# Kernel tuning notes

Measured on AMD Instinct MI355X. Metric: run time of the kernel, lower is better.

The kernel has to match this reference:

```python
import jax, jax.numpy as jnp
import numpy as np

EMBED_DIM = 1024
NUM_HEADS = 16
HEAD_DIM = EMBED_DIM // NUM_HEADS
SCALE = 1.0 / np.sqrt(HEAD_DIM)


def _quant_linear(x, w, b):
    # Per-tensor symmetric int8 quantize -> dequantize -> GEMM (faithful to QuantizedLinear)
    s = jnp.max(jnp.abs(w)) / 127.0
    w_dq = jnp.clip(jnp.round(w / s), -128.0, 127.0) * s
    return jnp.einsum('bse,oe->bso', x, w_dq) + b


def setup_inputs() -> dict:
    key = jax.random.key(0)
    ks = jax.random.split(key, 7)
    B, S, E = 2, 2048, EMBED_DIM
    return {
        'query': jax.random.normal(ks[0], (B, S, E), dtype=jnp.float32),
        'key': jax.random.normal(ks[1], (B, S, E), dtype=jnp.float32),
        'value': jax.random.normal(ks[2], (B, S, E), dtype=jnp.float32),
        'Wq': jax.random.normal(ks[3], (E, E), dtype=jnp.float32) * 0.02,
        'bq': jnp.zeros((E,), dtype=jnp.float32),
        'Wk': jax.random.normal(ks[4], (E, E), dtype=jnp.float32) * 0.02,
        'bk': jnp.zeros((E,), dtype=jnp.float32),
        'Wv': jax.random.normal(ks[5], (E, E), dtype=jnp.float32) * 0.02,
        'bv': jnp.zeros((E,), dtype=jnp.float32),
        'Wo': jax.random.normal(ks[6], (E, E), dtype=jnp.float32) * 0.02,
        'bo': jnp.zeros((E,), dtype=jnp.float32),
    }


def reference(query, key, value, Wq, bq, Wk, bk, Wv, bv, Wo, bo):
    B, S, E = query.shape
    H, D = NUM_HEADS, HEAD_DIM
    Q = _quant_linear(query, Wq, bq).reshape(B, S, H, D).transpose(0, 2, 1, 3)
    K = _quant_linear(key, Wk, bk).reshape(B, S, H, D).transpose(0, 2, 1, 3)
    V = _quant_linear(value, Wv, bv).reshape(B, S, H, D).transpose(0, 2, 1, 3)
    # [B,H,S,S] unfused attention scores
    scores = jnp.einsum('bhqd,bhkd->bhqk', Q, K) * SCALE
    attn = jax.nn.softmax(scores, axis=-1)  # dropout is identity at inference
    out = jnp.einsum('bhqk,bhkd->bhqd', attn, V)
    out = out.transpose(0, 2, 1, 3).reshape(B, S, E)
    return _quant_linear(out, Wo, bo)
```

## Files before the change

kernel.cpp:

```cpp
#include <hip/hip_runtime.h>
#include <math.h>

#define S_LEN 2048
#define EMB   1024
#define NHEAD 16
#define HDIM  64
#define MTOT  4096
#define EXP2_SCALE 0.18033688011112042f

typedef __attribute__((ext_vector_type(8))) short bf16x8;
typedef __attribute__((ext_vector_type(4))) float f32x4;

#if __has_builtin(__builtin_amdgcn_exp2f)
#define FEXP2(x) __builtin_amdgcn_exp2f(x)
#else
#define FEXP2(x) exp2f(x)
#endif

__device__ __forceinline__ short f2bf(float f) {
  union { float f; unsigned u; } v; v.f = f;
  unsigned r = v.u + 0x7fffu + ((v.u >> 16) & 1u);
  return (short)(r >> 16);
}
__device__ __forceinline__ float bf2f(short s) {
  union { float f; unsigned u; } v; v.u = ((unsigned)(unsigned short)s) << 16;
  return v.f;
}
__device__ __forceinline__ unsigned pkbf(float e0, float e1) {
  unsigned a = __float_as_uint(e1) + 0x8000u;
  unsigned b = __float_as_uint(e0) + 0x8000u;
  return __builtin_amdgcn_perm(a, b, 0x07060302u);
}

__device__ __forceinline__ void gload_lds16(const void* g, void* l) {
  __builtin_amdgcn_global_load_lds(
      (const __attribute__((address_space(1))) void*)g,
      (__attribute__((address_space(3))) void*)l, 16, 0, 0);
}

__global__ void wabsmax_k(const float* __restrict__ W0, const float* __restrict__ W1,
                          const float* __restrict__ W2, const float* __restrict__ W3,
                          unsigned* __restrict__ scaleU) {
  int w = blockIdx.x & 3;
  int part = blockIdx.x >> 2;
  const float* W = (w == 0) ? W0 : (w == 1) ? W1 : (w == 2) ? W2 : W3;
  float m = 0.f;
  int base = part * 16384;
#pragma unroll
  for (int p = 0; p < 16; ++p) {
    const float4 v = *(const float4*)&W[base + p * 1024 + threadIdx.x * 4];
    m = fmaxf(m, fmaxf(fmaxf(fabsf(v.x), fabsf(v.y)), fmaxf(fabsf(v.z), fabsf(v.w))));
  }
  __shared__ float red[256];
  red[threadIdx.x] = m;
  __syncthreads();
  for (int s = 128; s > 0; s >>= 1) {
    if (threadIdx.x < s) red[threadIdx.x] = fmaxf(red[threadIdx.x], red[threadIdx.x + s]);
    __syncthreads();
  }
  if (threadIdx.x == 0) atomicMax(&scaleU[w], __float_as_uint(red[0]));
}

__global__ void wquant_k(const float* __restrict__ W0, const float* __restrict__ W1,
                         const float* __restrict__ W2, const float* __restrict__ W3,
                         short* __restrict__ Q0, short* __restrict__ Q1,
                         short* __restrict__ Q2, short* __restrict__ Q3,
                         const unsigned* __restrict__ scaleU, float* __restrict__ sVal) {
  int w = blockIdx.y;
  const float* W = (w == 0) ? W0 : (w == 1) ? W1 : (w == 2) ? W2 : W3;
  short* Q = (w == 0) ? Q0 : (w == 1) ? Q1 : (w == 2) ? Q2 : Q3;
  float s = __uint_as_float(scaleU[w]) * (1.0f / 127.0f);
  if (blockIdx.x == 0 && threadIdx.x == 0) sVal[w] = s;
  int idx = (blockIdx.x * 256 + threadIdx.x) * 4;
  float4 v = *(const float4*)&W[idx];
  short4 q;
  q.x = f2bf(fminf(fmaxf(rintf(v.x / s), -128.f), 127.f));
  q.y = f2bf(fminf(fmaxf(rintf(v.y / s), -128.f), 127.f));
  q.z = f2bf(fminf(fmaxf(rintf(v.z / s), -128.f), 127.f));
  q.w = f2bf(fminf(fmaxf(rintf(v.w / s), -128.f), 127.f));
  *(short4*)&Q[idx] = q;
}

__global__ void acast_k(const float* __restrict__ A0, const float* __restrict__ A1,
                        const float* __restrict__ A2,
                        short* __restrict__ H0, short* __restrict__ H1,
                        short* __restrict__ H2) {
  int w = blockIdx.y;
  const float* A = (w == 0) ? A0 : (w == 1) ? A1 : A2;
  short* H = (w == 0) ? H0 : (w == 1) ? H1 : H2;
  int idx = (blockIdx.x * 256 + threadIdx.x) * 4;
  float4 v = *(const float4*)&A[idx];
  short4 h;
  h.x = f2bf(v.x); h.y = f2bf(v.y); h.z = f2bf(v.z); h.w = f2bf(v.w);
  *(short4*)&H[idx] = h;
}

__device__ __forceinline__ void gemm_core(
    const short* __restrict__ Ah, const short* __restrict__ Bq, int m0, int n0,
    short* AhS, short* BsS, f32x4 acc[4][4]) {
  const int tid = threadIdx.x;
  const int lane = tid & 63, wave = tid >> 6;
  const int quad = lane >> 4, l16 = lane & 15;
  const int wm = wave >> 1, wn = wave & 1;

  const int swrow = lane >> 2, swcol = (lane & 3) * 8;
  const short* agh = Ah + (m0 + wave * 32 + swrow) * 1024 + swcol;
  const short* bgp = Bq + (n0 + wave * 32 + swrow) * 1024 + swcol;
  short* sA0 = AhS + wave * 1024;
  short* sB0 = BsS + wave * 1024;

  for (int k0 = 0; k0 < 1024; k0 += 32) {
    __syncthreads();
    gload_lds16(agh + k0,             sA0);
    gload_lds16(agh + 16 * 1024 + k0, sA0 + 512);
    gload_lds16(bgp + k0,             sB0);
    gload_lds16(bgp + 16 * 1024 + k0, sB0 + 512);
    __syncthreads();
    bf16x8 ah[4], bb[4];
#pragma unroll
    for (int mi = 0; mi < 4; ++mi) {
      int row = wm * 64 + mi * 16 + l16;
      ah[mi] = *(const bf16x8*)&AhS[row * 32 + quad * 8];
    }
#pragma unroll
    for (int ni = 0; ni < 4; ++ni) {
      int row = wn * 64 + ni * 16 + l16;
      bb[ni] = *(const bf16x8*)&BsS[row * 32 + quad * 8];
    }
#pragma unroll
    for (int mi = 0; mi < 4; ++mi)
#pragma unroll
      for (int ni = 0; ni < 4; ++ni)
        acc[mi][ni] = __builtin_amdgcn_mfma_f32_16x16x32_bf16(ah[mi], bb[ni], acc[mi][ni], 0, 0, 0);
  }
}

__global__ __launch_bounds__(256, 2) void gemm_qkv(
    const short* __restrict__ QA, const short* __restrict__ KA, const short* __restrict__ VA,
    const short* __restrict__ WqQ, const short* __restrict__ WkQ, const short* __restrict__ WvQ,
    const float* __restrict__ sVal,
    const float* __restrict__ bq, const float* __restrict__ bk, const float* __restrict__ bv,
    short* __restrict__ Qh, short* __restrict__ Kh, short* __restrict__ Vh) {
  __shared__ __align__(16) short AhS[128 * 32];
  __shared__ __align__(16) short BsS[128 * 32];
  const int z = blockIdx.z;
  const short* Ah = (z == 0) ? QA : (z == 1) ? KA : VA;
  const short* Bq = (z == 0) ? WqQ : (z == 1) ? WkQ : WvQ;
  const float* bias = (z == 0) ? bq : (z == 1) ? bk : bv;
  short* oh = (z == 0) ? Qh : (z == 1) ? Kh : Vh;

  const int lin = blockIdx.y * 8 + blockIdx.x;
  const int map = (lin & 7) * 32 + (lin >> 3);
  const int m0 = (map >> 3) * 128, n0 = (map & 7) * 128;
  f32x4 acc[4][4];
#pragma unroll
  for (int i = 0; i < 4; ++i)
#pragma unroll
    for (int j = 0; j < 4; ++j) acc[i][j] = (f32x4){0.f, 0.f, 0.f, 0.f};

  gemm_core(Ah, Bq, m0, n0, AhS, BsS, acc);

  const int lane = threadIdx.x & 63, wave = threadIdx.x >> 6;
  const int quad = lane >> 4, l16 = lane & 15;
  const int wm = wave >> 1, wn = wave & 1;
  float s = sVal[z];
  float post = (z == 0) ? EXP2_SCALE : 1.0f;
#pragma unroll
  for (int mi = 0; mi < 4; ++mi) {
#pragma unroll
    for (int ni = 0; ni < 4; ++ni) {
      int rowb = m0 + wm * 64 + mi * 16 + quad * 4;
      int col = n0 + wn * 64 + ni * 16 + l16;
      float bia = bias[col];
      int h = col >> 6, d = col & 63;
      if (z < 2) {
#pragma unroll
        for (int r = 0; r < 4; ++r) {
          float v = (acc[mi][ni][r] * s + bia) * post;
          int row = rowb + r;
          int b = row >> 11, sq = row & 2047;
          oh[((b * 16 + h) * 2048 + sq) * 64 + d] = f2bf(v);
        }
      } else {
        int b = rowb >> 11, sq = rowb & 2047;
        short4 pk;
        pk.x = f2bf(acc[mi][ni][0] * s + bia);
        pk.y = f2bf(acc[mi][ni][1] * s + bia);
        pk.z = f2bf(acc[mi][ni][2] * s + bia);
        pk.w = f2bf(acc[mi][ni][3] * s + bia);
        *(short4*)&oh[((b * 16 + h) * 64 + d) * 2048 + sq] = pk;
      }
    }
  }
}

__global__ __launch_bounds__(256, 2) void gemm_o(
    const short* __restrict__ OAh, const short* __restrict__ OAl,
    const short* __restrict__ WoQ, const float* __restrict__ sPtr,
    const float* __restrict__ bias, float* __restrict__ outF) {
  __shared__ __align__(16) short AhS[128 * 32];
  __shared__ __align__(16) short AlS[128 * 32];
  __shared__ __align__(16) short BsS[64 * 32];
  const int tid = threadIdx.x;
  const int lane = tid & 63, wave = tid >> 6;
  const int quad = lane >> 4, l16 = lane & 15;
  const int lin = blockIdx.y * 16 + blockIdx.x;
  const int map = (lin & 7) * 64 + (lin >> 3);
  const int m0 = (map >> 4) * 128, n0 = (map & 15) * 64;

  f32x4 acc[2][4];
#pragma unroll
  for (int i = 0; i < 2; ++i)
#pragma unroll
    for (int j = 0; j < 4; ++j) acc[i][j] = (f32x4){0.f, 0.f, 0.f, 0.f};

  const int swrow = lane >> 2, swcol = (lane & 3) * 8;
  const short* agh = OAh + (m0 + wave * 32 + swrow) * 1024 + swcol;
  const short* agl = OAl + (m0 + wave * 32 + swrow) * 1024 + swcol;
  const short* bgp = WoQ + (n0 + wave * 16 + swrow) * 1024 + swcol;
  short* sA0 = AhS + wave * 1024;
  short* sA1 = AlS + wave * 1024;
  short* sB0 = BsS + wave * 512;

  for (int k0 = 0; k0 < 1024; k0 += 32) {
    __syncthreads();
    gload_lds16(agh + k0,             sA0);
    gload_lds16(agh + 16 * 1024 + k0, sA0 + 512);
    gload_lds16(agl + k0,             sA1);
    gload_lds16(agl + 16 * 1024 + k0, sA1 + 512);
    gload_lds16(bgp + k0,             sB0);
    __syncthreads();
    bf16x8 ah[2], al[2], bb[4];
#pragma unroll
    for (int mi = 0; mi < 2; ++mi) {
      int row = wave * 32 + mi * 16 + l16;
      ah[mi] = *(const bf16x8*)&AhS[row * 32 + quad * 8];
      al[mi] = *(const bf16x8*)&AlS[row * 32 + quad * 8];
    }
#pragma unroll
    for (int ni = 0; ni < 4; ++ni) {
      int row = ni * 16 + l16;
      bb[ni] = *(const bf16x8*)&BsS[row * 32 + quad * 8];
    }
#pragma unroll
    for (int mi = 0; mi < 2; ++mi)
#pragma unroll
      for (int ni = 0; ni < 4; ++ni) {
        acc[mi][ni] = __builtin_amdgcn_mfma_f32_16x16x32_bf16(ah[mi], bb[ni], acc[mi][ni], 0, 0, 0);
        acc[mi][ni] = __builtin_amdgcn_mfma_f32_16x16x32_bf16(al[mi], bb[ni], acc[mi][ni], 0, 0, 0);
      }
  }

  const float s = *sPtr;
#pragma unroll
  for (int mi = 0; mi < 2; ++mi) {
#pragma unroll
    for (int ni = 0; ni < 4; ++ni) {
      int rowb = m0 + wave * 32 + mi * 16 + quad * 4;
      int col = n0 + ni * 16 + l16;
      float bia = bias[col];
#pragma unroll
      for (int r = 0; r < 4; ++r)
        outF[(rowb + r) * 1024 + col] = acc[mi][ni][r] * s + bia;
    }
  }
}

__global__ __launch_bounds__(256, 2) void flash_k(
    const short* __restrict__ Qh, const short* __restrict__ Kh,
    const short* __restrict__ Vh,
    short* __restrict__ Ohi, short* __restrict__ Olo) {
  __shared__ __align__(16) short Khs[64 * 72];
  __shared__ __align__(16) short Vhs[64 * 72];

  const int tid = threadIdx.x;
  const int lane = tid & 63, wave = tid >> 6;
  const int quad = lane >> 4, l16 = lane & 15;
  const int bh = blockIdx.y;
  const int b = bh >> 4, h = bh & 15;
  const int q0 = blockIdx.x * 128 + wave * 32;
  const int qkbase = bh * (S_LEN * HDIM);
  const int vbase  = bh * (HDIM * S_LEN);

  bf16x8 qb[2][2];
#pragma unroll
  for (int g = 0; g < 2; ++g) {
    const int qrow = qkbase + (q0 + g * 16 + l16) * HDIM;
    qb[g][0] = *(const bf16x8*)&Qh[qrow + quad * 8];
    qb[g][1] = *(const bf16x8*)&Qh[qrow + 32 + quad * 8];
  }

  f32x4 zero = {0.f, 0.f, 0.f, 0.f};
  f32x4 oacc[2][4];
#pragma unroll
  for (int g = 0; g < 2; ++g)
#pragma unroll
    for (int i = 0; i < 4; ++i) oacc[g][i] = zero;
  f32x4 sacc[2] = {zero, zero};

  union { bf16x8 v; unsigned u[4]; } ones_;
  ones_.u[0] = ones_.u[1] = ones_.u[2] = ones_.u[3] = 0x3F803F80u;

  const int sr  = wave * 16 + l16;
  const int sc8 = quad * 8;
  const int srP = (sr & 32) | (((sr >> 2) & 1) << 4) | (((sr >> 3) & 3) << 2) | (sr & 3);
  const int kgl = qkbase + sr * HDIM + sc8;
  const int vgl = vbase + sr * S_LEN + sc8;
  const int kOff = srP * 72 + sc8;
  const int vOff = sr * 72 + sc8;

  bf16x8 pk0 = *(const bf16x8*)&Kh[kgl];
  bf16x8 pk1 = *(const bf16x8*)&Kh[kgl + 32];
  bf16x8 pv0 = *(const bf16x8*)&Vh[vgl];
  bf16x8 pv1 = *(const bf16x8*)&Vh[vgl + 32];

  for (int kt = 0; kt < S_LEN; kt += 64) {
    __syncthreads();
    *(bf16x8*)&Khs[kOff]      = pk0;
    *(bf16x8*)&Khs[kOff + 32] = pk1;
    *(bf16x8*)&Vhs[vOff]      = pv0;
    *(bf16x8*)&Vhs[vOff + 32] = pv1;
    __syncthreads();
    if (kt + 64 < S_LEN) {
      int kg = kgl + (kt + 64) * HDIM;
      int vg = vgl + (kt + 64);
      pk0 = *(const bf16x8*)&Kh[kg];
      pk1 = *(const bf16x8*)&Kh[kg + 32];
      pv0 = *(const bf16x8*)&Vh[vg];
      pv1 = *(const bf16x8*)&Vh[vg + 32];
    }
    f32x4 sc[2][4];
#pragma unroll
    for (int nj = 0; nj < 4; ++nj) {
      const int kr = nj * 16 + l16;
      bf16x8 kf0 = *(const bf16x8*)&Khs[kr * 72 + quad * 8];
      bf16x8 kf1 = *(const bf16x8*)&Khs[kr * 72 + 32 + quad * 8];
#pragma unroll
      for (int g = 0; g < 2; ++g) {
        f32x4 sv = zero;
        sv = __builtin_amdgcn_mfma_f32_16x16x32_bf16(kf0, qb[g][0], sv, 0, 0, 0);
        sv = __builtin_amdgcn_mfma_f32_16x16x32_bf16(kf1, qb[g][1], sv, 0, 0, 0);
        sc[g][nj] = sv;
      }
    }
#pragma unroll
    for (int g = 0; g < 2; ++g)
#pragma unroll
      for (int nj = 0; nj < 4; ++nj)
#pragma unroll
        for (int r = 0; r < 4; ++r)
          sc[g][nj][r] = FEXP2(sc[g][nj][r]);
    union { bf16x8 v; unsigned u[4]; } P[2][2];
#pragma unroll
    for (int g = 0; g < 2; ++g) {
      P[g][0].u[0] = pkbf(sc[g][0][0], sc[g][0][1]);
      P[g][0].u[1] = pkbf(sc[g][0][2], sc[g][0][3]);
      P[g][0].u[2] = pkbf(sc[g][1][0], sc[g][1][1]);
      P[g][0].u[3] = pkbf(sc[g][1][2], sc[g][1][3]);
      P[g][1].u[0] = pkbf(sc[g][2][0], sc[g][2][1]);
      P[g][1].u[1] = pkbf(sc[g][2][2], sc[g][2][3]);
      P[g][1].u[2] = pkbf(sc[g][3][0], sc[g][3][1]);
      P[g][1].u[3] = pkbf(sc[g][3][2], sc[g][3][3]);
    }
#pragma unroll
    for (int g = 0; g < 2; ++g) {
      sacc[g] = __builtin_amdgcn_mfma_f32_16x16x32_bf16(P[g][0].v, ones_.v, sacc[g], 0, 0, 0);
      sacc[g] = __builtin_amdgcn_mfma_f32_16x16x32_bf16(P[g][1].v, ones_.v, sacc[g], 0, 0, 0);
    }
#pragma unroll
    for (int ni = 0; ni < 4; ++ni) {
      int vr = ni * 16 + l16;
      bf16x8 vf0 = *(const bf16x8*)&Vhs[vr * 72 + quad * 8];
      bf16x8 vf1 = *(const bf16x8*)&Vhs[vr * 72 + 32 + quad * 8];
#pragma unroll
      for (int g = 0; g < 2; ++g) {
        oacc[g][ni] = __builtin_amdgcn_mfma_f32_16x16x32_bf16(P[g][0].v, vf0, oacc[g][ni], 0, 0, 0);
        oacc[g][ni] = __builtin_amdgcn_mfma_f32_16x16x32_bf16(P[g][1].v, vf1, oacc[g][ni], 0, 0, 0);
      }
    }
  }
#pragma unroll
  for (int g = 0; g < 2; ++g) {
#pragma unroll
    for (int r = 0; r < 4; ++r) {
      float inv = 1.f / sacc[g][r];
      int row = b * S_LEN + q0 + g * 16 + quad * 4 + r;
#pragma unroll
      for (int ni = 0; ni < 4; ++ni) {
        float v = oacc[g][ni][r] * inv;
        int idx = row * 1024 + h * 64 + ni * 16 + l16;
        short hi = f2bf(v);
        Ohi[idx] = hi;
        Olo[idx] = f2bf(v - bf2f(hi));
      }
    }
  }
}

extern "C" void kernel_launch(void* const* d_in, const int* in_sizes, int n_in,
                              void* d_out, int out_size, void* d_ws, size_t ws_size,
                              hipStream_t stream) {
  const float* query = (const float*)d_in[0];
  const float* key_i = (const float*)d_in[1];
  const float* value = (const float*)d_in[2];
  const float* Wq = (const float*)d_in[3];
  const float* bq = (const float*)d_in[4];
  const float* Wk = (const float*)d_in[5];
  const float* bk = (const float*)d_in[6];
  const float* Wv = (const float*)d_in[7];
  const float* bv = (const float*)d_in[8];
  const float* Wo = (const float*)d_in[9];
  const float* bo = (const float*)d_in[10];
  float* out = (float*)d_out;

  char* w = (char*)d_ws;
  unsigned* scaleU = (unsigned*)w;
  float* sVal = (float*)(w + 256);
  size_t off = 512;
  const size_t SZ_W = 2097152;
  const size_t SZ_A = 8388608;
  short* WqQ = (short*)(w + off); off += SZ_W;
  short* WkQ = (short*)(w + off); off += SZ_W;
  short* WvQ = (short*)(w + off); off += SZ_W;
  short* WoQ = (short*)(w + off); off += SZ_W;
  short* Qa  = (short*)(w + off); off += SZ_A;
  short* Ka  = (short*)(w + off); off += SZ_A;
  short* Va  = (short*)(w + off); off += SZ_A;
  short* Qh  = (short*)(w + off); off += SZ_A;
  short* Kh  = (short*)(w + off); off += SZ_A;
  short* Vh  = (short*)(w + off); off += SZ_A;
  short* Ohi = Qa;
  short* Olo = Ka;

  (void)hipMemsetAsync(scaleU, 0, 16, stream);
  wabsmax_k<<<256, 256, 0, stream>>>(Wq, Wk, Wv, Wo, scaleU);
  wquant_k<<<dim3(1024, 4), 256, 0, stream>>>(Wq, Wk, Wv, Wo, WqQ, WkQ, WvQ, WoQ, scaleU, sVal);
  acast_k<<<dim3(4096, 3), 256, 0, stream>>>(query, key_i, value, Qa, Ka, Va);
  gemm_qkv<<<dim3(8, 32, 3), 256, 0, stream>>>(Qa, Ka, Va, WqQ, WkQ, WvQ, sVal,
                                               bq, bk, bv, Qh, Kh, Vh);
  flash_k<<<dim3(16, 32), 256, 0, stream>>>(Qh, Kh, Vh, Ohi, Olo);
  gemm_o<<<dim3(16, 32), 256, 0, stream>>>(Ohi, Olo, WoQ, sVal + 3, bo, out);
}
```

Measured before the change: 233.3 us.

## Load K fragments directly from global into registers and remap block order

The flash attention kernel stops staging K through shared memory. Each lane instead loads its K MFMA fragments straight from global memory into double-buffered register sets, unrolling the loop by two tiles, and only V still goes through LDS. The block index is also remapped so that neighbouring blocks work on different heads, which is meant to spread L2 and cache traffic. This cuts LDS writes and reads for K, but every wave now re-reads K from global or L2 and register pressure goes up.

```diff
diff --git a/kernel.cpp b/kernel.cpp
--- a/kernel.cpp
+++ b/kernel.cpp
@@ -266,19 +266,95 @@
   }
 }
 
+#define MF(a, b, c) __builtin_amdgcn_mfma_f32_16x16x32_bf16(a, b, c, 0, 0, 0)
+
+#define FLASH_TILE(KF, KN, ktv)                                               \
+  {                                                                           \
+    __syncthreads();                                                          \
+    *(bf16x8*)&Vhs[vOff]      = pv0;                                          \
+    *(bf16x8*)&Vhs[vOff + 32] = pv1;                                          \
+    __syncthreads();                                                          \
+    const int ktn = (ktv) + 64;                                               \
+    if (ktn < S_LEN) {                                                        \
+      pv0 = *(const bf16x8*)&Vh[vgl + ktn];                                   \
+      pv1 = *(const bf16x8*)&Vh[vgl + ktn + 32];                              \
+      const int ko = ktn * HDIM;                                              \
+      KN##0 = *(const bf16x8*)&kp0[ko]; KN##1 = *(const bf16x8*)&kp0[ko + 32];\
+      KN##2 = *(const bf16x8*)&kp1[ko]; KN##3 = *(const bf16x8*)&kp1[ko + 32];\
+      KN##4 = *(const bf16x8*)&kp2[ko]; KN##5 = *(const bf16x8*)&kp2[ko + 32];\
+      KN##6 = *(const bf16x8*)&kp3[ko]; KN##7 = *(const bf16x8*)&kp3[ko + 32];\
+    }                                                                         \
+    f32x4 sc[2][4];                                                           \
+    {                                                                         \
+      f32x4 sv;                                                               \
+      sv = zero; sv = MF(KF##0, qb[0][0], sv); sv = MF(KF##1, qb[0][1], sv);  \
+      sc[0][0] = sv;                                                          \
+      sv = zero; sv = MF(KF##0, qb[1][0], sv); sv = MF(KF##1, qb[1][1], sv);  \
+      sc[1][0] = sv;                                                          \
+      sv = zero; sv = MF(KF##2, qb[0][0], sv); sv = MF(KF##3, qb[0][1], sv);  \
+      sc[0][1] = sv;                                                          \
+      sv = zero; sv = MF(KF##2, qb[1][0], sv); sv = MF(KF##3, qb[1][1], sv);  \
+      sc[1][1] = sv;                                                          \
+      sv = zero; sv = MF(KF##4, qb[0][0], sv); sv = MF(KF##5, qb[0][1], sv);  \
+      sc[0][2] = sv;                                                          \
+      sv = zero; sv = MF(KF##4, qb[1][0], sv); sv = MF(KF##5, qb[1][1], sv);  \
+      sc[1][2] = sv;                                                          \
+      sv = zero; sv = MF(KF##6, qb[0][0], sv); sv = MF(KF##7, qb[0][1], sv);  \
+      sc[0][3] = sv;                                                          \
+      sv = zero; sv = MF(KF##6, qb[1][0], sv); sv = MF(KF##7, qb[1][1], sv);  \
+      sc[1][3] = sv;                                                          \
+    }                                                                         \
+    _Pragma("unroll")                                                         \
+    for (int g = 0; g < 2; ++g)                                               \
+      _Pragma("unroll")                                                       \
+      for (int nj = 0; nj < 4; ++nj)                                          \
+        _Pragma("unroll")                                                     \
+        for (int r = 0; r < 4; ++r)                                           \
+          sc[g][nj][r] = FEXP2(sc[g][nj][r]);                                 \
+    union { bf16x8 v; unsigned u[4]; } P[2][2];                               \
+    _Pragma("unroll")                                                         \
+    for (int g = 0; g < 2; ++g) {                                             \
+      P[g][0].u[0] = pkbf(sc[g][0][0], sc[g][0][1]);                          \
+      P[g][0].u[1] = pkbf(sc[g][0][2], sc[g][0][3]);                          \
+      P[g][0].u[2] = pkbf(sc[g][1][0], sc[g][1][1]);                          \
+      P[g][0].u[3] = pkbf(sc[g][1][2], sc[g][1][3]);                          \
+      P[g][1].u[0] = pkbf(sc[g][2][0], sc[g][2][1]);                          \
+      P[g][1].u[1] = pkbf(sc[g][2][2], sc[g][2][3]);                          \
+      P[g][1].u[2] = pkbf(sc[g][3][0], sc[g][3][1]);                          \
+      P[g][1].u[3] = pkbf(sc[g][3][2], sc[g][3][3]);                          \
+    }                                                                         \
+    _Pragma("unroll")                                                         \
+    for (int g = 0; g < 2; ++g) {                                             \
+      sacc[g] = MF(P[g][0].v, ones_.v, sacc[g]);                              \
+      sacc[g] = MF(P[g][1].v, ones_.v, sacc[g]);                              \
+    }                                                                         \
+    _Pragma("unroll")                                                         \
+    for (int ni = 0; ni < 4; ++ni) {                                          \
+      int vr = ni * 16 + l16;                                                 \
+      bf16x8 vf0 = *(const bf16x8*)&Vhs[vr * 72 + quad * 8];                  \
+      bf16x8 vf1 = *(const bf16x8*)&Vhs[vr * 72 + 32 + quad * 8];             \
+      _Pragma("unroll")                                                       \
+      for (int g = 0; g < 2; ++g) {                                           \
+        oacc[g][ni] = MF(P[g][0].v, vf0, oacc[g][ni]);                        \
+        oacc[g][ni] = MF(P[g][1].v, vf1, oacc[g][ni]);                        \
+      }                                                                       \
+    }                                                                         \
+  }
+
 __global__ __launch_bounds__(256, 2) void flash_k(
     const short* __restrict__ Qh, const short* __restrict__ Kh,
     const short* __restrict__ Vh,
     short* __restrict__ Ohi, short* __restrict__ Olo) {
-  __shared__ __align__(16) short Khs[64 * 72];
   __shared__ __align__(16) short Vhs[64 * 72];
 
   const int tid = threadIdx.x;
   const int lane = tid & 63, wave = tid >> 6;
   const int quad = lane >> 4, l16 = lane & 15;
-  const int bh = blockIdx.y;
+  const int lin = blockIdx.y * 16 + blockIdx.x;
+  const int map = (lin & 7) * 64 + (lin >> 3);
+  const int bh = map >> 4;
   const int b = bh >> 4, h = bh & 15;
-  const int q0 = blockIdx.x * 128 + wave * 32;
+  const int q0 = (map & 15) * 128 + wave * 32;
   const int qkbase = bh * (S_LEN * HDIM);
   const int vbase  = bh * (HDIM * S_LEN);
 
@@ -303,81 +379,27 @@
 
   const int sr  = wave * 16 + l16;
   const int sc8 = quad * 8;
-  const int srP = (sr & 32) | (((sr >> 2) & 1) << 4) | (((sr >> 3) & 3) << 2) | (sr & 3);
-  const int kgl = qkbase + sr * HDIM + sc8;
-  const int vgl = vbase + sr * S_LEN + sc8;
-  const int kOff = srP * 72 + sc8;
+  const int vgl  = vbase + sr * S_LEN + sc8;
   const int vOff = sr * 72 + sc8;
 
-  bf16x8 pk0 = *(const bf16x8*)&Kh[kgl];
-  bf16x8 pk1 = *(const bf16x8*)&Kh[kgl + 32];
+  const int rbase = (l16 & 3) | ((l16 & 12) << 1);
+  const short* kp0 = Kh + qkbase + (rbase | 0 ) * HDIM + quad * 8;
+  const short* kp1 = Kh + qkbase + (rbase | 4 ) * HDIM + quad * 8;
+  const short* kp2 = Kh + qkbase + (rbase | 32) * HDIM + quad * 8;
+  const short* kp3 = Kh + qkbase + (rbase | 36) * HDIM + quad * 8;
+
   bf16x8 pv0 = *(const bf16x8*)&Vh[vgl];
   bf16x8 pv1 = *(const bf16x8*)&Vh[vgl + 32];
-
-  for (int kt = 0; kt < S_LEN; kt += 64) {
-    __syncthreads();
-    *(bf16x8*)&Khs[kOff]      = pk0;
-    *(bf16x8*)&Khs[kOff + 32] = pk1;
-    *(bf16x8*)&Vhs[vOff]      = pv0;
-    *(bf16x8*)&Vhs[vOff + 32] = pv1;
-    __syncthreads();
-    if (kt + 64 < S_LEN) {
-      int kg = kgl + (kt + 64) * HDIM;
-      int vg = vgl + (kt + 64);
-      pk0 = *(const bf16x8*)&Kh[kg];
-      pk1 = *(const bf16x8*)&Kh[kg + 32];
-      pv0 = *(const bf16x8*)&Vh[vg];
-      pv1 = *(const bf16x8*)&Vh[vg + 32];
-    }
-    f32x4 sc[2][4];
-#pragma unroll
-    for (int nj = 0; nj < 4; ++nj) {
-      const int kr = nj * 16 + l16;
-      bf16x8 kf0 = *(const bf16x8*)&Khs[kr * 72 + quad * 8];
-      bf16x8 kf1 = *(const bf16x8*)&Khs[kr * 72 + 32 + quad * 8];
-#pragma unroll
-      for (int g = 0; g < 2; ++g) {
-        f32x4 sv = zero;
-        sv = __builtin_amdgcn_mfma_f32_16x16x32_bf16(kf0, qb[g][0], sv, 0, 0, 0);
-        sv = __builtin_amdgcn_mfma_f32_16x16x32_bf16(kf1, qb[g][1], sv, 0, 0, 0);
-        sc[g][nj] = sv;
-      }
-    }
-#pragma unroll
-    for (int g = 0; g < 2; ++g)
-#pragma unroll
-      for (int nj = 0; nj < 4; ++nj)
-#pragma unroll
-        for (int r = 0; r < 4; ++r)
-          sc[g][nj][r] = FEXP2(sc[g][nj][r]);
-    union { bf16x8 v; unsigned u[4]; } P[2][2];
-#pragma unroll
-    for (int g = 0; g < 2; ++g) {
-      P[g][0].u[0] = pkbf(sc[g][0][0], sc[g][0][1]);
-      P[g][0].u[1] = pkbf(sc[g][0][2], sc[g][0][3]);
-      P[g][0].u[2] = pkbf(sc[g][1][0], sc[g][1][1]);
-      P[g][0].u[3] = pkbf(sc[g][1][2], sc[g][1][3]);
-      P[g][1].u[0] = pkbf(sc[g][2][0], sc[g][2][1]);
-      P[g][1].u[1] = pkbf(sc[g][2][2], sc[g][2][3]);
-      P[g][1].u[2] = pkbf(sc[g][3][0], sc[g][3][1]);
-      P[g][1].u[3] = pkbf(sc[g][3][2], sc[g][3][3]);
-    }
-#pragma unroll
-    for (int g = 0; g < 2; ++g) {
-      sacc[g] = __builtin_amdgcn_mfma_f32_16x16x32_bf16(P[g][0].v, ones_.v, sacc[g], 0, 0, 0);
-      sacc[g] = __builtin_amdgcn_mfma_f32_16x16x32_bf16(P[g][1].v, ones_.v, sacc[g], 0, 0, 0);
-    }
-#pragma unroll
-    for (int ni = 0; ni < 4; ++ni) {
-      int vr = ni * 16 + l16;
-      bf16x8 vf0 = *(const bf16x8*)&Vhs[vr * 72 + quad * 8];
-      bf16x8 vf1 = *(const bf16x8*)&Vhs[vr * 72 + 32 + quad * 8];
-#pragma unroll
-      for (int g = 0; g < 2; ++g) {
-        oacc[g][ni] = __builtin_amdgcn_mfma_f32_16x16x32_bf16(P[g][0].v, vf0, oacc[g][ni], 0, 0, 0);
-        oacc[g][ni] = __builtin_amdgcn_mfma_f32_16x16x32_bf16(P[g][1].v, vf1, oacc[g][ni], 0, 0, 0);
-      }
-    }
+  bf16x8 kA0 = *(const bf16x8*)&kp0[0], kA1 = *(const bf16x8*)&kp0[32];
+  bf16x8 kA2 = *(const bf16x8*)&kp1[0], kA3 = *(const bf16x8*)&kp1[32];
+  bf16x8 kA4 = *(const bf16x8*)&kp2[0], kA5 = *(const bf16x8*)&kp2[32];
+  bf16x8 kA6 = *(const bf16x8*)&kp3[0], kA7 = *(const bf16x8*)&kp3[32];
+  bf16x8 kB0 = kA0, kB1 = kA1, kB2 = kA2, kB3 = kA3;
+  bf16x8 kB4 = kA4, kB5 = kA5, kB6 = kA6, kB7 = kA7;
+
+  for (int kt = 0; kt < S_LEN; kt += 128) {
+    FLASH_TILE(kA, kB, kt)
+    FLASH_TILE(kB, kA, kt + 64)
   }
 #pragma unroll
   for (int g = 0; g < 2; ++g) {
```

New measurement: 270.0 us. 1.16x slower.

## Halve flash attention block size, double grid, and remap blocks for XCD locality

Applied to the files above, without the earlier changes.

The flash attention kernel now runs 128-thread blocks of 2 waves, each covering 64 query rows, over a 32x32 grid instead of 256-thread blocks over 16x32. The K/V tile loader is rewritten so each of the 128 threads loads half a row as four 16-byte vectors. Block indices are remapped so that blocks launched in round-robin across chiplets end up sharing the same (batch, head), which is meant to improve L2 reuse of K/V. Smaller blocks give more blocks for load balance, but each K/V tile staged in shared memory is now reused by fewer waves.

```diff
diff --git a/kernel.cpp b/kernel.cpp
--- a/kernel.cpp
+++ b/kernel.cpp
@@ -266,7 +266,7 @@
   }
 }
 
-__global__ __launch_bounds__(256, 2) void flash_k(
+__global__ __launch_bounds__(128, 2) void flash_k(
     const short* __restrict__ Qh, const short* __restrict__ Kh,
     const short* __restrict__ Vh,
     short* __restrict__ Ohi, short* __restrict__ Olo) {
@@ -276,9 +276,11 @@
   const int tid = threadIdx.x;
   const int lane = tid & 63, wave = tid >> 6;
   const int quad = lane >> 4, l16 = lane & 15;
-  const int bh = blockIdx.y;
+  const int lin = blockIdx.y * 32 + blockIdx.x;
+  const int map = (lin & 7) * 128 + (lin >> 3);
+  const int bh = map >> 5;
   const int b = bh >> 4, h = bh & 15;
-  const int q0 = blockIdx.x * 128 + wave * 32;
+  const int q0 = (map & 31) * 64 + wave * 32;
   const int qkbase = bh * (S_LEN * HDIM);
   const int vbase  = bh * (HDIM * S_LEN);
 
@@ -301,33 +303,45 @@
   union { bf16x8 v; unsigned u[4]; } ones_;
   ones_.u[0] = ones_.u[1] = ones_.u[2] = ones_.u[3] = 0x3F803F80u;
 
-  const int sr  = wave * 16 + l16;
-  const int sc8 = quad * 8;
+  const int sr  = tid >> 1;
+  const int c2  = (tid & 1) * 32;
   const int srP = (sr & 32) | (((sr >> 2) & 1) << 4) | (((sr >> 3) & 3) << 2) | (sr & 3);
-  const int kgl = qkbase + sr * HDIM + sc8;
-  const int vgl = vbase + sr * S_LEN + sc8;
-  const int kOff = srP * 72 + sc8;
-  const int vOff = sr * 72 + sc8;
+  const int kgl = qkbase + sr * HDIM + c2;
+  const int vgl = vbase + sr * S_LEN + c2;
+  const int kOff = srP * 72 + c2;
+  const int vOff = sr * 72 + c2;
 
   bf16x8 pk0 = *(const bf16x8*)&Kh[kgl];
-  bf16x8 pk1 = *(const bf16x8*)&Kh[kgl + 32];
+  bf16x8 pk1 = *(const bf16x8*)&Kh[kgl + 8];
+  bf16x8 pk2 = *(const bf16x8*)&Kh[kgl + 16];
+  bf16x8 pk3 = *(const bf16x8*)&Kh[kgl + 24];
   bf16x8 pv0 = *(const bf16x8*)&Vh[vgl];
-  bf16x8 pv1 = *(const bf16x8*)&Vh[vgl + 32];
+  bf16x8 pv1 = *(const bf16x8*)&Vh[vgl + 8];
+  bf16x8 pv2 = *(const bf16x8*)&Vh[vgl + 16];
+  bf16x8 pv3 = *(const bf16x8*)&Vh[vgl + 24];
 
   for (int kt = 0; kt < S_LEN; kt += 64) {
     __syncthreads();
     *(bf16x8*)&Khs[kOff]      = pk0;
-    *(bf16x8*)&Khs[kOff + 32] = pk1;
+    *(bf16x8*)&Khs[kOff + 8]  = pk1;
+    *(bf16x8*)&Khs[kOff + 16] = pk2;
+    *(bf16x8*)&Khs[kOff + 24] = pk3;
     *(bf16x8*)&Vhs[vOff]      = pv0;
-    *(bf16x8*)&Vhs[vOff + 32] = pv1;
+    *(bf16x8*)&Vhs[vOff + 8]  = pv1;
+    *(bf16x8*)&Vhs[vOff + 16] = pv2;
+    *(bf16x8*)&Vhs[vOff + 24] = pv3;
     __syncthreads();
     if (kt + 64 < S_LEN) {
       int kg = kgl + (kt + 64) * HDIM;
       int vg = vgl + (kt + 64);
       pk0 = *(const bf16x8*)&Kh[kg];
-      pk1 = *(const bf16x8*)&Kh[kg + 32];
+      pk1 = *(const bf16x8*)&Kh[kg + 8];
+      pk2 = *(const bf16x8*)&Kh[kg + 16];
+      pk3 = *(const bf16x8*)&Kh[kg + 24];
       pv0 = *(const bf16x8*)&Vh[vg];
-      pv1 = *(const bf16x8*)&Vh[vg + 32];
+      pv1 = *(const bf16x8*)&Vh[vg + 8];
+      pv2 = *(const bf16x8*)&Vh[vg + 16];
+      pv3 = *(const bf16x8*)&Vh[vg + 24];
     }
     f32x4 sc[2][4];
 #pragma unroll
@@ -438,6 +452,6 @@
   acast_k<<<dim3(4096, 3), 256, 0, stream>>>(query, key_i, value, Qa, Ka, Va);
   gemm_qkv<<<dim3(8, 32, 3), 256, 0, stream>>>(Qa, Ka, Va, WqQ, WkQ, WvQ, sVal,
                                                bq, bk, bv, Qh, Kh, Vh);
-  flash_k<<<dim3(16, 32), 256, 0, stream>>>(Qh, Kh, Vh, Ohi, Olo);
+  flash_k<<<dim3(32, 32), 128, 0, stream>>>(Qh, Kh, Vh, Ohi, Olo);
   gemm_o<<<dim3(16, 32), 256, 0, stream>>>(Ohi, Olo, WoQ, sVal + 3, bo, out);
 }
```

Result: slower. 238.7 us (+2.3%).
